# Optimization experiments

Measured on AMD Instinct MI355X. Metric: run time of the kernel, lower is better.

Reference implementation:

```python
import jax, jax.numpy as jnp
import numpy as np

TEMP = 5.0

def setup_inputs() -> dict:
    key = jax.random.key(0)
    k1, k2 = jax.random.split(key)
    text_features = jax.random.normal(k1, (512, 512), dtype=jnp.float32)   # [A, D]
    video_features = jax.random.normal(k2, (512, 32, 512), dtype=jnp.float32)  # [B, V, D]
    return {"text_features": text_features, "video_features": video_features}

def reference(text_features, video_features):
    # scores: [A, B, V] = text (A,D) x video (B,V,D)
    v_weight = jnp.einsum('ad,bvd->abv', text_features, video_features)
    v_weight = jax.nn.softmax(v_weight / TEMP, axis=-1)
    # pooled: [A, B, D]
    v_feat = jnp.einsum('abv,bvd->abd', v_weight, video_features)
    return v_feat
```

## Files before the change

### kernel.cpp

```cpp
#include <hip/hip_runtime.h>

typedef _Float16 f16x8 __attribute__((ext_vector_type(8)));
typedef _Float16 f16x4 __attribute__((ext_vector_type(4)));
typedef float f32x4 __attribute__((ext_vector_type(4)));

#define NA 512
#define NB 512
#define NV 32
#define ND 512
#define NBV (NB * NV)

__global__ __launch_bounds__(256) void k_prep(const float* __restrict__ text,
                                              const float* __restrict__ video,
                                              _Float16* __restrict__ Tf,
                                              _Float16* __restrict__ Vf,
                                              _Float16* __restrict__ VT) {
  __shared__ _Float16 tile[ND * NV];
  int b = blockIdx.x, t = threadIdx.x;
  const float* vb = video + (size_t)b * NV * ND;
  int v = t >> 3, dc = (t & 7) * 64;
  for (int i = 0; i < 16; ++i) {
    f32x4 x = *(const f32x4*)(vb + v * ND + dc + i * 4);
    int d = dc + i * 4;
    tile[(d + 0) * NV + v] = (_Float16)x[0];
    tile[(d + 1) * NV + v] = (_Float16)x[1];
    tile[(d + 2) * NV + v] = (_Float16)x[2];
    tile[(d + 3) * NV + v] = (_Float16)x[3];
  }
  for (int i = 0; i < 16; ++i) {
    int off = i * 1024 + t * 4;
    f32x4 x = *(const f32x4*)(vb + off);
    f16x4 h;
    h[0] = (_Float16)x[0]; h[1] = (_Float16)x[1];
    h[2] = (_Float16)x[2]; h[3] = (_Float16)x[3];
    *(f16x4*)(Vf + (size_t)b * (NV * ND) + off) = h;
  }
  if (b < 256) {
    int idx = (b * 256 + t) * 4;
    f32x4 x = *(const f32x4*)(text + idx);
    f16x4 h;
    h[0] = (_Float16)x[0]; h[1] = (_Float16)x[1];
    h[2] = (_Float16)x[2]; h[3] = (_Float16)x[3];
    *(f16x4*)(Tf + idx) = h;
  }
  __syncthreads();
  f16x8* dst = (f16x8*)(VT + (size_t)b * ND * NV);
  const f16x8* src = (const f16x8*)tile;
  for (int i = 0; i < 8; ++i) dst[i * 256 + t] = src[i * 256 + t];
}

__device__ inline int swz(int row, int ch) {
  return row * 32 + ((ch ^ ((row >> 1) & 3)) * 8);
}

__global__ __launch_bounds__(256) void k_scores(const _Float16* __restrict__ Tf,
                                                const _Float16* __restrict__ Vf,
                                                _Float16* __restrict__ W) {
  __shared__ _Float16 As[64 * 32];
  __shared__ _Float16 Bs[128 * 32];
  int t = threadIdx.x;
  int m0 = blockIdx.y * 64, n0 = blockIdx.x * 128;
  int w = t >> 6, lane = t & 63, ln = lane & 15, q = lane >> 4;
  int wm = (w >> 1) * 32, wn = (w & 1) * 64;
  int ra = t >> 2, ca = t & 3;
  int rb = t >> 1, cb = (t & 1) * 2;
  const _Float16* tA = Tf + (size_t)(m0 + ra) * ND + ca * 8;
  const _Float16* tB = Vf + (size_t)(n0 + rb) * ND + cb * 8;
  f32x4 acc[2][4];
  for (int i = 0; i < 2; ++i)
    for (int j = 0; j < 4; ++j) acc[i][j] = (f32x4){0.f, 0.f, 0.f, 0.f};

  for (int kk = 0; kk < 16; ++kk) {
    int k0 = kk * 32;
    __syncthreads();
    *(f16x8*)(As + swz(ra, ca)) = *(const f16x8*)(tA + k0);
    *(f16x8*)(Bs + swz(rb, cb)) = *(const f16x8*)(tB + k0);
    *(f16x8*)(Bs + swz(rb, cb + 1)) = *(const f16x8*)(tB + k0 + 8);
    __syncthreads();
    f16x8 af[2], bf[4];
    for (int mt = 0; mt < 2; ++mt)
      af[mt] = *(const f16x8*)(As + swz(wm + mt * 16 + ln, q));
    for (int nt = 0; nt < 4; ++nt)
      bf[nt] = *(const f16x8*)(Bs + swz(wn + nt * 16 + ln, q));
    for (int mt = 0; mt < 2; ++mt)
      for (int nt = 0; nt < 4; ++nt)
        acc[mt][nt] = __builtin_amdgcn_mfma_f32_16x16x32_f16(af[mt], bf[nt],
                                                             acc[mt][nt], 0, 0, 0);
  }

  const float invT = 0.2f;
  for (int mt = 0; mt < 2; ++mt) {
    for (int g = 0; g < 2; ++g) {
      for (int r = 0; r < 4; ++r) {
        float v0 = acc[mt][2 * g][r] * invT;
        float v1 = acc[mt][2 * g + 1][r] * invT;
        float mx = fmaxf(v0, v1);
        for (int msk = 1; msk < 16; msk <<= 1)
          mx = fmaxf(mx, __shfl_xor(mx, msk, 16));
        float p0 = __expf(v0 - mx), p1 = __expf(v1 - mx);
        float s = p0 + p1;
        for (int msk = 1; msk < 16; msk <<= 1)
          s += __shfl_xor(s, msk, 16);
        float inv = 1.0f / s;
        int a = m0 + wm + mt * 16 + q * 4 + r;
        int col = n0 + wn + g * 32 + ln;
        W[(size_t)a * NBV + col] = (_Float16)(p0 * inv);
        W[(size_t)a * NBV + col + 16] = (_Float16)(p1 * inv);
      }
    }
  }
}

__global__ __launch_bounds__(512) void k_pool(const _Float16* __restrict__ W,
                                              const _Float16* __restrict__ VT,
                                              float* __restrict__ out) {
  int t = threadIdx.x;
  int w = t >> 6, lane = t & 63, ln = lane & 15, q = lane >> 4;
  int b0 = blockIdx.x * 8, a0 = blockIdx.y * 64;
  int d0 = w * 64;
  const _Float16* Wbase = W + (size_t)(a0 + ln) * NBV + b0 * NV + q * 8;
  for (int ib = 0; ib < 8; ++ib) {
    const _Float16* vtb =
        VT + ((size_t)(b0 + ib) * ND + d0 + ln) * NV + q * 8;
    f16x8 wf[4], vf[4];
    for (int nt = 0; nt < 4; ++nt)
      wf[nt] = *(const f16x8*)(Wbase + (size_t)nt * 16 * NBV + ib * NV);
    for (int mt = 0; mt < 4; ++mt)
      vf[mt] = *(const f16x8*)(vtb + mt * 16 * NV);
    for (int nt = 0; nt < 4; ++nt) {
      for (int mt = 0; mt < 4; ++mt) {
        f32x4 c = (f32x4){0.f, 0.f, 0.f, 0.f};
        c = __builtin_amdgcn_mfma_f32_16x16x32_f16(vf[mt], wf[nt], c, 0, 0, 0);
        float* dst = out + ((size_t)(a0 + nt * 16 + ln) * NB + b0 + ib) * ND +
                     d0 + mt * 16 + q * 4;
        *(f32x4*)dst = c;
      }
    }
  }
}

extern "C" void kernel_launch(void* const* d_in, const int* in_sizes, int n_in,
                              void* d_out, int out_size, void* d_ws, size_t ws_size,
                              hipStream_t stream) {
  const float* text = (const float*)d_in[0];
  const float* video = (const float*)d_in[1];
  float* out = (float*)d_out;
  _Float16* ws = (_Float16*)d_ws;
  _Float16* VT = ws;
  _Float16* W  = ws + (size_t)8 * 1024 * 1024;
  _Float16* Vf = ws + (size_t)16 * 1024 * 1024;
  _Float16* Tf = ws + (size_t)24 * 1024 * 1024;
  k_prep<<<dim3(NB), 256, 0, stream>>>(text, video, Tf, Vf, VT);
  k_scores<<<dim3(NBV / 128, NA / 64), 256, 0, stream>>>(Tf, Vf, W);
  k_pool<<<dim3(NB / 8, NA / 64), 512, 0, stream>>>(W, VT, out);
}
```

Baseline: 633.1 us.

## Switch pooling stage to fp32 FMA with fp32 softmax weights, drop transposed fp16 video

Removes the transposed fp16 video copy from the prep kernel and stores the softmax weights as fp32 instead of fp16. The pooling kernel is rewritten to use scalar fp32 FMAs on the original video tensor held in registers instead of MFMA, with one block per video and group of 64 text rows. This likely targets accuracy, or the cost of the shared-memory transpose and the poor MFMA use in pooling. It doubles the weight traffic (32 MB fp32) and moves the pooling math onto plain vector ALUs.

```diff
diff --git a/kernel.cpp b/kernel.cpp
--- a/kernel.cpp
+++ b/kernel.cpp
@@ -13,27 +13,17 @@
 __global__ __launch_bounds__(256) void k_prep(const float* __restrict__ text,
                                               const float* __restrict__ video,
                                               _Float16* __restrict__ Tf,
-                                              _Float16* __restrict__ Vf,
-                                              _Float16* __restrict__ VT) {
-  __shared__ _Float16 tile[ND * NV];
+                                              _Float16* __restrict__ Vf) {
   int b = blockIdx.x, t = threadIdx.x;
   const float* vb = video + (size_t)b * NV * ND;
-  int v = t >> 3, dc = (t & 7) * 64;
-  for (int i = 0; i < 16; ++i) {
-    f32x4 x = *(const f32x4*)(vb + v * ND + dc + i * 4);
-    int d = dc + i * 4;
-    tile[(d + 0) * NV + v] = (_Float16)x[0];
-    tile[(d + 1) * NV + v] = (_Float16)x[1];
-    tile[(d + 2) * NV + v] = (_Float16)x[2];
-    tile[(d + 3) * NV + v] = (_Float16)x[3];
-  }
+  _Float16* ob = Vf + (size_t)b * NV * ND;
   for (int i = 0; i < 16; ++i) {
     int off = i * 1024 + t * 4;
     f32x4 x = *(const f32x4*)(vb + off);
     f16x4 h;
     h[0] = (_Float16)x[0]; h[1] = (_Float16)x[1];
     h[2] = (_Float16)x[2]; h[3] = (_Float16)x[3];
-    *(f16x4*)(Vf + (size_t)b * (NV * ND) + off) = h;
+    *(f16x4*)(ob + off) = h;
   }
   if (b < 256) {
     int idx = (b * 256 + t) * 4;
@@ -43,10 +33,6 @@
     h[2] = (_Float16)x[2]; h[3] = (_Float16)x[3];
     *(f16x4*)(Tf + idx) = h;
   }
-  __syncthreads();
-  f16x8* dst = (f16x8*)(VT + (size_t)b * ND * NV);
-  const f16x8* src = (const f16x8*)tile;
-  for (int i = 0; i < 8; ++i) dst[i * 256 + t] = src[i * 256 + t];
 }
 
 __device__ inline int swz(int row, int ch) {
@@ -55,7 +41,7 @@
 
 __global__ __launch_bounds__(256) void k_scores(const _Float16* __restrict__ Tf,
                                                 const _Float16* __restrict__ Vf,
-                                                _Float16* __restrict__ W) {
+                                                float* __restrict__ Wf) {
   __shared__ _Float16 As[64 * 32];
   __shared__ _Float16 Bs[128 * 32];
   int t = threadIdx.x;
@@ -104,37 +90,43 @@
         float inv = 1.0f / s;
         int a = m0 + wm + mt * 16 + q * 4 + r;
         int col = n0 + wn + g * 32 + ln;
-        W[(size_t)a * NBV + col] = (_Float16)(p0 * inv);
-        W[(size_t)a * NBV + col + 16] = (_Float16)(p1 * inv);
+        Wf[(size_t)a * NBV + col] = p0 * inv;
+        Wf[(size_t)a * NBV + col + 16] = p1 * inv;
       }
     }
   }
 }
 
-__global__ __launch_bounds__(512) void k_pool(const _Float16* __restrict__ W,
-                                              const _Float16* __restrict__ VT,
+__global__ __launch_bounds__(256) void k_pool(const float* __restrict__ Wf,
+                                              const float* __restrict__ video,
                                               float* __restrict__ out) {
-  int t = threadIdx.x;
-  int w = t >> 6, lane = t & 63, ln = lane & 15, q = lane >> 4;
-  int b0 = blockIdx.x * 8, a0 = blockIdx.y * 64;
-  int d0 = w * 64;
-  const _Float16* Wbase = W + (size_t)(a0 + ln) * NBV + b0 * NV + q * 8;
-  for (int ib = 0; ib < 8; ++ib) {
-    const _Float16* vtb =
-        VT + ((size_t)(b0 + ib) * ND + d0 + ln) * NV + q * 8;
-    f16x8 wf[4], vf[4];
-    for (int nt = 0; nt < 4; ++nt)
-      wf[nt] = *(const f16x8*)(Wbase + (size_t)nt * 16 * NBV + ib * NV);
-    for (int mt = 0; mt < 4; ++mt)
-      vf[mt] = *(const f16x8*)(vtb + mt * 16 * NV);
-    for (int nt = 0; nt < 4; ++nt) {
-      for (int mt = 0; mt < 4; ++mt) {
-        f32x4 c = (f32x4){0.f, 0.f, 0.f, 0.f};
-        c = __builtin_amdgcn_mfma_f32_16x16x32_f16(vf[mt], wf[nt], c, 0, 0, 0);
-        float* dst = out + ((size_t)(a0 + nt * 16 + ln) * NB + b0 + ib) * ND +
-                     d0 + mt * 16 + q * 4;
-        *(f32x4*)dst = c;
+  int b = blockIdx.x, t = threadIdx.x;
+  int w = t >> 6, lane = t & 63;
+  int a0 = blockIdx.y * 64 + w * 16;
+  const float* vb = video + (size_t)b * NV * ND;
+  for (int c = 0; c < 2; ++c) {
+    f32x4 vr[32];
+#pragma unroll
+    for (int v = 0; v < 32; ++v)
+      vr[v] = *(const f32x4*)(vb + (size_t)v * ND + c * 256 + lane * 4);
+    for (int i = 0; i < 16; ++i) {
+      int a = a0 + i;
+      const f32x4* wrow = (const f32x4*)(Wf + (size_t)a * NBV + b * NV);
+      f32x4 s = (f32x4){0.f, 0.f, 0.f, 0.f};
+#pragma unroll
+      for (int k = 0; k < 8; ++k) {
+        f32x4 wv = wrow[k];
+#pragma unroll
+        for (int e = 0; e < 4; ++e) {
+          float wgt = wv[e];
+          int v = k * 4 + e;
+          s[0] = fmaf(wgt, vr[v][0], s[0]);
+          s[1] = fmaf(wgt, vr[v][1], s[1]);
+          s[2] = fmaf(wgt, vr[v][2], s[2]);
+          s[3] = fmaf(wgt, vr[v][3], s[3]);
+        }
       }
+      *(f32x4*)(out + ((size_t)a * NB + b) * ND + c * 256 + lane * 4) = s;
     }
   }
 }
@@ -145,12 +137,10 @@
   const float* text = (const float*)d_in[0];
   const float* video = (const float*)d_in[1];
   float* out = (float*)d_out;
-  _Float16* ws = (_Float16*)d_ws;
-  _Float16* VT = ws;
-  _Float16* W  = ws + (size_t)8 * 1024 * 1024;
-  _Float16* Vf = ws + (size_t)16 * 1024 * 1024;
-  _Float16* Tf = ws + (size_t)24 * 1024 * 1024;
-  k_prep<<<dim3(NB), 256, 0, stream>>>(text, video, Tf, Vf, VT);
-  k_scores<<<dim3(NBV / 128, NA / 64), 256, 0, stream>>>(Tf, Vf, W);
-  k_pool<<<dim3(NB / 8, NA / 64), 512, 0, stream>>>(W, VT, out);
+  float* Wf = (float*)d_ws;
+  _Float16* Vf = (_Float16*)((char*)d_ws + (size_t)32 * 1024 * 1024);
+  _Float16* Tf = (_Float16*)((char*)d_ws + (size_t)48 * 1024 * 1024);
+  k_prep<<<dim3(NB), 256, 0, stream>>>(text, video, Tf, Vf);
+  k_scores<<<dim3(NBV / 128, NA / 64), 256, 0, stream>>>(Tf, Vf, Wf);
+  k_pool<<<dim3(NB, NA / 64), 256, 0, stream>>>(Wf, video, out);
 }
```

After: 718.9 us. +13.5%, slower.
